# Kernel optimization log

Hardware: AMD Instinct MI355X
Metric: run time of the kernel (lower is better)

## Reference

```python
import jax, jax.numpy as jnp
import numpy as np

DIM0, DIMO, WIDTH, DEPTH = 64, 16, 128, 6  # depth = number of weight matrices
N = 524288


def setup_inputs() -> dict:
    key = jax.random.key(0)
    ks = jax.random.split(key, DEPTH + 1)
    x = jax.random.normal(ks[0], (N, DIM0), dtype=jnp.float32)
    bd0 = 1.0 / np.sqrt(DIM0)   # first layer init bound (per torch code)
    bd = 1.0 / np.sqrt(WIDTH)   # remaining layers init bound
    W0 = jax.random.uniform(ks[1], (DIM0, WIDTH), minval=-bd0, maxval=bd0, dtype=jnp.float32)
    W1 = jax.random.uniform(ks[2], (WIDTH, WIDTH), minval=-bd, maxval=bd, dtype=jnp.float32)
    W2 = jax.random.uniform(ks[3], (WIDTH, WIDTH), minval=-bd, maxval=bd, dtype=jnp.float32)
    W3 = jax.random.uniform(ks[4], (WIDTH, WIDTH), minval=-bd, maxval=bd, dtype=jnp.float32)
    W4 = jax.random.uniform(ks[5], (WIDTH, WIDTH), minval=-bd, maxval=bd, dtype=jnp.float32)
    W5 = jax.random.uniform(ks[6], (WIDTH, DIMO), minval=-bd, maxval=bd, dtype=jnp.float32)
    bias = jnp.zeros((DIMO,), dtype=jnp.float32)
    return {"x": x, "W0": W0, "W1": W1, "W2": W2, "W3": W3, "W4": W4, "W5": W5, "bias": bias}


def reference(x, W0, W1, W2, W3, W4, W5, bias):
    # Fully-fused MLP math: matmul (no bias) + ReLU for every layer except the
    # last (output_activation='None'); then cast back to x dtype and add bias.
    h = jax.nn.relu(x @ W0)
    h = jax.nn.relu(h @ W1)
    h = jax.nn.relu(h @ W2)
    h = jax.nn.relu(h @ W3)
    h = jax.nn.relu(h @ W4)
    out = (h @ W5).astype(x.dtype) + bias
    return out
```

## Files before the change

### kernel.cpp

```cpp
#include <hip/hip_runtime.h>
#include <stdint.h>


typedef __bf16 bf16x8 __attribute__((ext_vector_type(8)));
typedef __bf16 bf16x4 __attribute__((ext_vector_type(4)));
typedef float  floatx4 __attribute__((ext_vector_type(4)));

constexpr int NS   = 524288;
constexpr int TILE = 64;
constexpr int NBLK = NS / TILE;

constexpr int WTOT = 9472;

__global__ void prep_weights(const float* __restrict__ W0, const float* __restrict__ W1,
                             const float* __restrict__ W2, const float* __restrict__ W3,
                             const float* __restrict__ W4, const float* __restrict__ W5,
                             bf16x8* __restrict__ ws) {
  int gid = blockIdx.x * blockDim.x + threadIdx.x;
  if (gid >= WTOT) return;
  const float* Wsrc; int nout, kt_n, base;
  if (gid < 1024)      { Wsrc = W0; nout = 128; kt_n = 2; base = 0;    }
  else if (gid < 3072) { Wsrc = W1; nout = 128; kt_n = 4; base = 1024; }
  else if (gid < 5120) { Wsrc = W2; nout = 128; kt_n = 4; base = 3072; }
  else if (gid < 7168) { Wsrc = W3; nout = 128; kt_n = 4; base = 5120; }
  else if (gid < 9216) { Wsrc = W4; nout = 128; kt_n = 4; base = 7168; }
  else                 { Wsrc = W5; nout = 16;  kt_n = 4; base = 9216; }
  int id   = gid - base;
  int lane = id & 63;
  int frag = id >> 6;
  int kt   = frag % kt_n;
  int rb   = frag / kt_n;
  int row   = rb * 16 + (lane & 15);
  int chunk = kt * 4 + (lane >> 4);
  bf16x8 v;
#pragma unroll
  for (int j = 0; j < 8; ++j)
    v[j] = (__bf16)Wsrc[(8 * chunk + j) * nout + row];
  ws[gid] = v;
}

__device__ __forceinline__ void zero_acc(floatx4 acc[4][4]) {
  floatx4 z = {0.f, 0.f, 0.f, 0.f};
#pragma unroll
  for (int i = 0; i < 4; ++i)
#pragma unroll
    for (int j = 0; j < 4; ++j) acc[i][j] = z;
}

template <int KT>
__device__ __forceinline__ void layer_mm(const bf16x8* __restrict__ Wg, const bf16x8* Hb,
                                         floatx4 acc[4][4], int w, int lane, int l15, int g) {
#pragma unroll
  for (int kt = 0; kt < KT; ++kt) {
    const int cx = (kt * 4 + g) ^ (l15 & 7);
    bf16x8 a[4], b[4];
#pragma unroll
    for (int i = 0; i < 4; ++i)
      a[i] = Wg[((4 * w + i) * KT + kt) * 64 + lane];
#pragma unroll
    for (int i = 0; i < 4; ++i) b[i] = Hb[(16 * i + l15) * 16 + cx];
#pragma unroll
    for (int ot = 0; ot < 4; ++ot)
#pragma unroll
      for (int nt = 0; nt < 4; ++nt)
        acc[ot][nt] = __builtin_amdgcn_mfma_f32_16x16x32_bf16(a[ot], b[nt], acc[ot][nt], 0, 0, 0);
  }
}

__device__ __forceinline__ void write_h(bf16x4* H8, const floatx4 acc[4][4],
                                        int m_base, int l15, int g) {
#pragma unroll
  for (int ot = 0; ot < 4; ++ot) {
    int ob    = m_base + 16 * ot + 4 * g;
    int phys8 = (((ob >> 3) ^ (l15 & 7)) << 1) | ((ob >> 2) & 1);
#pragma unroll
    for (int nt = 0; nt < 4; ++nt) {
      int s = 16 * nt + l15;
      floatx4 v = acc[ot][nt];
      bf16x4 h;
      h[0] = (__bf16)fmaxf(v[0], 0.0f);
      h[1] = (__bf16)fmaxf(v[1], 0.0f);
      h[2] = (__bf16)fmaxf(v[2], 0.0f);
      h[3] = (__bf16)fmaxf(v[3], 0.0f);
      H8[s * 32 + phys8] = h;
    }
  }
}

__global__ void __launch_bounds__(128, 3) mlp_kernel(const float* __restrict__ x,
                                                     const float* __restrict__ bias,
                                                     const bf16x8* __restrict__ wimg,
                                                     float* __restrict__ out) {
  __shared__ bf16x8 Hbuf[2 * TILE * 16];

  bf16x8* H0 = Hbuf;
  bf16x8* H1 = Hbuf + TILE * 16;

  const int t    = threadIdx.x;
  const int lane = t & 63;
  const int w    = t >> 6;
  const int l15  = lane & 15;
  const int g    = lane >> 4;
  const int m_base = w * 64;
  const int tile = blockIdx.x;

  constexpr int WOFF[6] = {0, 1024, 3072, 5120, 7168, 9216};

  const float* xt = x + (size_t)tile * TILE * 64;
#pragma unroll
  for (int i = 0; i < 4; ++i) {
    int f2 = t + 128 * i;
    int s = f2 >> 3, c = f2 & 7;
    const floatx4* src = (const floatx4*)(xt + f2 * 8);
    floatx4 lo = src[0], hi = src[1];
    bf16x8 v;
    v[0] = (__bf16)lo[0]; v[1] = (__bf16)lo[1]; v[2] = (__bf16)lo[2]; v[3] = (__bf16)lo[3];
    v[4] = (__bf16)hi[0]; v[5] = (__bf16)hi[1]; v[6] = (__bf16)hi[2]; v[7] = (__bf16)hi[3];
    H0[s * 16 + (c ^ (s & 7))] = v;
  }
  __syncthreads();

  floatx4 acc[4][4];

  zero_acc(acc);
  layer_mm<2>(wimg + WOFF[0], H0, acc, w, lane, l15, g);
  write_h((bf16x4*)H1, acc, m_base, l15, g);
  __syncthreads();

#pragma unroll
  for (int l = 1; l <= 4; ++l) {
    const bf16x8* Hr = (l & 1) ? H1 : H0;
    bf16x4*       Hw = (l & 1) ? (bf16x4*)H0 : (bf16x4*)H1;
    zero_acc(acc);
    layer_mm<4>(wimg + WOFF[l], Hr, acc, w, lane, l15, g);
    write_h(Hw, acc, m_base, l15, g);
    __syncthreads();
  }

  const bf16x8* W5g = wimg + WOFF[5];
  floatx4 a5[2];
  {
    floatx4 z = {0.f, 0.f, 0.f, 0.f};
    a5[0] = z; a5[1] = z;
  }
  const int n5 = w * 32;
#pragma unroll
  for (int kt = 0; kt < 4; ++kt) {
    int cx = (kt * 4 + g) ^ (l15 & 7);
    bf16x8 a = W5g[kt * 64 + lane];
#pragma unroll
    for (int nt = 0; nt < 2; ++nt) {
      bf16x8 b = H1[(n5 + 16 * nt + l15) * 16 + cx];
      a5[nt] = __builtin_amdgcn_mfma_f32_16x16x32_bf16(a, b, a5[nt], 0, 0, 0);
    }
  }
  floatx4 bv = *(const floatx4*)(bias + 4 * g);
  floatx4* outv = (floatx4*)out;
#pragma unroll
  for (int nt = 0; nt < 2; ++nt) {
    int s = tile * TILE + n5 + 16 * nt + l15;
    outv[s * 4 + g] = a5[nt] + bv;
  }
}

extern "C" void kernel_launch(void* const* d_in, const int* in_sizes, int n_in,
                              void* d_out, int out_size, void* d_ws, size_t ws_size,
                              hipStream_t stream) {
  (void)in_sizes; (void)n_in; (void)out_size; (void)ws_size;
  const float* x    = (const float*)d_in[0];
  const float* W0   = (const float*)d_in[1];
  const float* W1   = (const float*)d_in[2];
  const float* W2   = (const float*)d_in[3];
  const float* W3   = (const float*)d_in[4];
  const float* W4   = (const float*)d_in[5];
  const float* W5   = (const float*)d_in[6];
  const float* bias = (const float*)d_in[7];
  bf16x8* ws = (bf16x8*)d_ws;

  prep_weights<<<(WTOT + 255) / 256, 256, 0, stream>>>(W0, W1, W2, W3, W4, W5, ws);
  mlp_kernel<<<NBLK, 128, 0, stream>>>(x, bias, (const bf16x8*)ws, (float*)d_out);
}
```

Before: 269.7 us.

## Keep MLP activations in registers with permuted weight layout, drop shared memory

Each wave now owns 64 samples and computes all 128 output features itself. The MFMA accumulator layout is repacked directly into the B operand of the next layer, with the input-feature permutation (kappa) folded into the prepped weight image. This removes the LDS round trip and the __syncthreads between layers. In exchange each wave loads every weight fragment from global/L2 for only 64 samples instead of sharing them, and register pressure rises (acc[8][4] plus B[4][4]), with launch bounds changed to 256 threads and 2 blocks.

```diff
diff --git a/kernel.cpp b/kernel.cpp
--- a/kernel.cpp
+++ b/kernel.cpp
@@ -3,14 +3,17 @@
 
 
 typedef __bf16 bf16x8 __attribute__((ext_vector_type(8)));
-typedef __bf16 bf16x4 __attribute__((ext_vector_type(4)));
 typedef float  floatx4 __attribute__((ext_vector_type(4)));
 
-constexpr int NS   = 524288;
-constexpr int TILE = 64;
-constexpr int NBLK = NS / TILE;
+constexpr int NS    = 524288;
+constexpr int SPW   = 64;
+constexpr int NBLK  = NS / (SPW * 4);
 
 constexpr int WTOT = 9472;
+
+__device__ __host__ __forceinline__ int kappa(int s) {
+  return 32 * (s >> 5) + 16 * ((s >> 2) & 1) + 4 * ((s >> 3) & 3) + (s & 3);
+}
 
 __global__ void prep_weights(const float* __restrict__ W0, const float* __restrict__ W1,
                              const float* __restrict__ W2, const float* __restrict__ W3,
@@ -18,148 +21,127 @@
                              bf16x8* __restrict__ ws) {
   int gid = blockIdx.x * blockDim.x + threadIdx.x;
   if (gid >= WTOT) return;
-  const float* Wsrc; int nout, kt_n, base;
-  if (gid < 1024)      { Wsrc = W0; nout = 128; kt_n = 2; base = 0;    }
-  else if (gid < 3072) { Wsrc = W1; nout = 128; kt_n = 4; base = 1024; }
-  else if (gid < 5120) { Wsrc = W2; nout = 128; kt_n = 4; base = 3072; }
-  else if (gid < 7168) { Wsrc = W3; nout = 128; kt_n = 4; base = 5120; }
-  else if (gid < 9216) { Wsrc = W4; nout = 128; kt_n = 4; base = 7168; }
-  else                 { Wsrc = W5; nout = 16;  kt_n = 4; base = 9216; }
+  const float* Wsrc; int nout, kt_n, base, ident;
+  if (gid < 1024)      { Wsrc = W0; nout = 128; kt_n = 2; base = 0;    ident = 1; }
+  else if (gid < 3072) { Wsrc = W1; nout = 128; kt_n = 4; base = 1024; ident = 0; }
+  else if (gid < 5120) { Wsrc = W2; nout = 128; kt_n = 4; base = 3072; ident = 0; }
+  else if (gid < 7168) { Wsrc = W3; nout = 128; kt_n = 4; base = 5120; ident = 0; }
+  else if (gid < 9216) { Wsrc = W4; nout = 128; kt_n = 4; base = 7168; ident = 0; }
+  else                 { Wsrc = W5; nout = 16;  kt_n = 4; base = 9216; ident = 0; }
   int id   = gid - base;
   int lane = id & 63;
   int frag = id >> 6;
   int kt   = frag % kt_n;
   int rb   = frag / kt_n;
-  int row   = rb * 16 + (lane & 15);
-  int chunk = kt * 4 + (lane >> 4);
+  int outf = rb * 16 + (lane & 15);
+  int gg   = lane >> 4;
   bf16x8 v;
 #pragma unroll
-  for (int j = 0; j < 8; ++j)
-    v[j] = (__bf16)Wsrc[(8 * chunk + j) * nout + row];
+  for (int e = 0; e < 8; ++e) {
+    int s  = 32 * kt + 8 * gg + e;
+    int in = ident ? s : kappa(s);
+    v[e] = (__bf16)Wsrc[in * nout + outf];
+  }
   ws[gid] = v;
 }
 
-__device__ __forceinline__ void zero_acc(floatx4 acc[4][4]) {
+__device__ __forceinline__ void zero_acc(floatx4 acc[8][4]) {
   floatx4 z = {0.f, 0.f, 0.f, 0.f};
 #pragma unroll
-  for (int i = 0; i < 4; ++i)
+  for (int ot = 0; ot < 8; ++ot)
 #pragma unroll
-    for (int j = 0; j < 4; ++j) acc[i][j] = z;
+    for (int i = 0; i < 4; ++i) acc[ot][i] = z;
 }
 
-template <int KT>
-__device__ __forceinline__ void layer_mm(const bf16x8* __restrict__ Wg, const bf16x8* Hb,
-                                         floatx4 acc[4][4], int w, int lane, int l15, int g) {
+__device__ __forceinline__ void pack_relu(const floatx4 acc[8][4], bf16x8 B[4][4]) {
 #pragma unroll
-  for (int kt = 0; kt < KT; ++kt) {
-    const int cx = (kt * 4 + g) ^ (l15 & 7);
-    bf16x8 a[4], b[4];
+  for (int kt = 0; kt < 4; ++kt)
 #pragma unroll
-    for (int i = 0; i < 4; ++i)
-      a[i] = Wg[((4 * w + i) * KT + kt) * 64 + lane];
-#pragma unroll
-    for (int i = 0; i < 4; ++i) b[i] = Hb[(16 * i + l15) * 16 + cx];
-#pragma unroll
-    for (int ot = 0; ot < 4; ++ot)
-#pragma unroll
-      for (int nt = 0; nt < 4; ++nt)
-        acc[ot][nt] = __builtin_amdgcn_mfma_f32_16x16x32_bf16(a[ot], b[nt], acc[ot][nt], 0, 0, 0);
-  }
+    for (int i = 0; i < 4; ++i) {
+      floatx4 u = acc[2 * kt][i], v = acc[2 * kt + 1][i];
+      bf16x8 b;
+      b[0] = (__bf16)fmaxf(u[0], 0.f); b[1] = (__bf16)fmaxf(u[1], 0.f);
+      b[2] = (__bf16)fmaxf(u[2], 0.f); b[3] = (__bf16)fmaxf(u[3], 0.f);
+      b[4] = (__bf16)fmaxf(v[0], 0.f); b[5] = (__bf16)fmaxf(v[1], 0.f);
+      b[6] = (__bf16)fmaxf(v[2], 0.f); b[7] = (__bf16)fmaxf(v[3], 0.f);
+      B[kt][i] = b;
+    }
 }
 
-__device__ __forceinline__ void write_h(bf16x4* H8, const floatx4 acc[4][4],
-                                        int m_base, int l15, int g) {
-#pragma unroll
-  for (int ot = 0; ot < 4; ++ot) {
-    int ob    = m_base + 16 * ot + 4 * g;
-    int phys8 = (((ob >> 3) ^ (l15 & 7)) << 1) | ((ob >> 2) & 1);
-#pragma unroll
-    for (int nt = 0; nt < 4; ++nt) {
-      int s = 16 * nt + l15;
-      floatx4 v = acc[ot][nt];
-      bf16x4 h;
-      h[0] = (__bf16)fmaxf(v[0], 0.0f);
-      h[1] = (__bf16)fmaxf(v[1], 0.0f);
-      h[2] = (__bf16)fmaxf(v[2], 0.0f);
-      h[3] = (__bf16)fmaxf(v[3], 0.0f);
-      H8[s * 32 + phys8] = h;
-    }
-  }
-}
-
-__global__ void __launch_bounds__(128, 3) mlp_kernel(const float* __restrict__ x,
+__global__ void __launch_bounds__(256, 2) mlp_kernel(const float* __restrict__ x,
                                                      const float* __restrict__ bias,
                                                      const bf16x8* __restrict__ wimg,
                                                      float* __restrict__ out) {
-  __shared__ bf16x8 Hbuf[2 * TILE * 16];
-
-  bf16x8* H0 = Hbuf;
-  bf16x8* H1 = Hbuf + TILE * 16;
-
   const int t    = threadIdx.x;
   const int lane = t & 63;
   const int w    = t >> 6;
   const int l15  = lane & 15;
   const int g    = lane >> 4;
-  const int m_base = w * 64;
-  const int tile = blockIdx.x;
+  const size_t sbase = ((size_t)blockIdx.x * 4 + w) * SPW;
 
-  constexpr int WOFF[6] = {0, 1024, 3072, 5120, 7168, 9216};
+  bf16x8  B[4][4];
+  floatx4 acc[8][4];
 
-  const float* xt = x + (size_t)tile * TILE * 64;
+  const float* xw = x + sbase * 64;
 #pragma unroll
-  for (int i = 0; i < 4; ++i) {
-    int f2 = t + 128 * i;
-    int s = f2 >> 3, c = f2 & 7;
-    const floatx4* src = (const floatx4*)(xt + f2 * 8);
-    floatx4 lo = src[0], hi = src[1];
-    bf16x8 v;
-    v[0] = (__bf16)lo[0]; v[1] = (__bf16)lo[1]; v[2] = (__bf16)lo[2]; v[3] = (__bf16)lo[3];
-    v[4] = (__bf16)hi[0]; v[5] = (__bf16)hi[1]; v[6] = (__bf16)hi[2]; v[7] = (__bf16)hi[3];
-    H0[s * 16 + (c ^ (s & 7))] = v;
-  }
-  __syncthreads();
-
-  floatx4 acc[4][4];
+  for (int kt = 0; kt < 2; ++kt)
+#pragma unroll
+    for (int i = 0; i < 4; ++i) {
+      const floatx4* p = (const floatx4*)(xw + (16 * i + l15) * 64 + 32 * kt + 8 * g);
+      floatx4 lo = p[0], hi = p[1];
+      bf16x8 v;
+      v[0] = (__bf16)lo[0]; v[1] = (__bf16)lo[1]; v[2] = (__bf16)lo[2]; v[3] = (__bf16)lo[3];
+      v[4] = (__bf16)hi[0]; v[5] = (__bf16)hi[1]; v[6] = (__bf16)hi[2]; v[7] = (__bf16)hi[3];
+      B[kt][i] = v;
+    }
 
   zero_acc(acc);
-  layer_mm<2>(wimg + WOFF[0], H0, acc, w, lane, l15, g);
-  write_h((bf16x4*)H1, acc, m_base, l15, g);
-  __syncthreads();
+#pragma unroll
+  for (int kt = 0; kt < 2; ++kt)
+#pragma unroll
+    for (int ot = 0; ot < 8; ++ot) {
+      bf16x8 a = wimg[(ot * 2 + kt) * 64 + lane];
+#pragma unroll
+      for (int i = 0; i < 4; ++i)
+        acc[ot][i] = __builtin_amdgcn_mfma_f32_16x16x32_bf16(a, B[kt][i], acc[ot][i], 0, 0, 0);
+    }
 
+  constexpr int WOFFH[4] = {1024, 3072, 5120, 7168};
 #pragma unroll
-  for (int l = 1; l <= 4; ++l) {
-    const bf16x8* Hr = (l & 1) ? H1 : H0;
-    bf16x4*       Hw = (l & 1) ? (bf16x4*)H0 : (bf16x4*)H1;
+  for (int l = 0; l < 4; ++l) {
+    pack_relu(acc, B);
     zero_acc(acc);
-    layer_mm<4>(wimg + WOFF[l], Hr, acc, w, lane, l15, g);
-    write_h(Hw, acc, m_base, l15, g);
-    __syncthreads();
+    const bf16x8* Wl = wimg + WOFFH[l];
+#pragma unroll
+    for (int kt = 0; kt < 4; ++kt)
+#pragma unroll
+      for (int ot = 0; ot < 8; ++ot) {
+        bf16x8 a = Wl[(ot * 4 + kt) * 64 + lane];
+#pragma unroll
+        for (int i = 0; i < 4; ++i)
+          acc[ot][i] = __builtin_amdgcn_mfma_f32_16x16x32_bf16(a, B[kt][i], acc[ot][i], 0, 0, 0);
+      }
   }
 
-  const bf16x8* W5g = wimg + WOFF[5];
-  floatx4 a5[2];
+  pack_relu(acc, B);
+  floatx4 o[4];
   {
     floatx4 z = {0.f, 0.f, 0.f, 0.f};
-    a5[0] = z; a5[1] = z;
+    o[0] = z; o[1] = z; o[2] = z; o[3] = z;
   }
-  const int n5 = w * 32;
 #pragma unroll
   for (int kt = 0; kt < 4; ++kt) {
-    int cx = (kt * 4 + g) ^ (l15 & 7);
-    bf16x8 a = W5g[kt * 64 + lane];
+    bf16x8 a = wimg[9216 + kt * 64 + lane];
 #pragma unroll
-    for (int nt = 0; nt < 2; ++nt) {
-      bf16x8 b = H1[(n5 + 16 * nt + l15) * 16 + cx];
-      a5[nt] = __builtin_amdgcn_mfma_f32_16x16x32_bf16(a, b, a5[nt], 0, 0, 0);
-    }
+    for (int i = 0; i < 4; ++i)
+      o[i] = __builtin_amdgcn_mfma_f32_16x16x32_bf16(a, B[kt][i], o[i], 0, 0, 0);
   }
   floatx4 bv = *(const floatx4*)(bias + 4 * g);
   floatx4* outv = (floatx4*)out;
 #pragma unroll
-  for (int nt = 0; nt < 2; ++nt) {
-    int s = tile * TILE + n5 + 16 * nt + l15;
-    outv[s * 4 + g] = a5[nt] + bv;
+  for (int i = 0; i < 4; ++i) {
+    size_t s = sbase + 16 * i + l15;
+    outv[s * 4 + g] = o[i] + bv;
   }
 }
 
@@ -178,5 +160,5 @@
   bf16x8* ws = (bf16x8*)d_ws;
 
   prep_weights<<<(WTOT + 255) / 256, 256, 0, stream>>>(W0, W1, W2, W3, W4, W5, ws);
-  mlp_kernel<<<NBLK, 128, 0, stream>>>(x, bias, (const bf16x8*)ws, (float*)d_out);
+  mlp_kernel<<<NBLK, 256, 0, stream>>>(x, bias, (const bf16x8*)ws, (float*)d_out);
 }
```

Measured after the change: 335.1 us. 24.3% more time.
